# Kernel optimization log

Hardware: AMD Instinct MI355X
Metric: run time of the kernel (lower is better)

Reference implementation:

```python
import math
import jax, jax.numpy as jnp
import numpy as np

NH, D, MULT, VOCAB, NLAYER = 4, 256, 128, 256, 2
N = MULT * D // NH  # 8192
EPS = 1e-5
THETA = 2.0 ** 16


def get_freqs(n):
    q = (jnp.arange(n, dtype=jnp.float32) // 2) * 2  # quantize(t, 2)
    return 1.0 / (THETA ** (q / n)) / (2 * math.pi)


def ln(x):
    # LayerNorm over last dim, no affine
    mu = jnp.mean(x, axis=-1, keepdims=True)
    var = jnp.mean((x - mu) ** 2, axis=-1, keepdims=True)
    return (x - mu) / jnp.sqrt(var + EPS)


def rope(phases, v):
    # phases: (T, N), v: (B, nh, T, N)
    ph = (phases % 1.0) * (2 * math.pi)
    c, s = jnp.cos(ph), jnp.sin(ph)
    v_rot = jnp.stack((-v[..., 1::2], v[..., ::2]), axis=-1).reshape(v.shape)
    return v * c + v_rot * s


def setup_inputs() -> dict:
    key = jax.random.key(0)
    ks = jax.random.split(key, 6)
    std = 0.02
    return {
        "idx": jax.random.randint(ks[0], (1, 2048), 0, VOCAB),
        "embed": jax.random.normal(ks[1], (VOCAB, D), jnp.float32) * std,
        "encoder": jax.random.normal(ks[2], (NH, D, N), jnp.float32) * std,
        "encoder_v": jax.random.normal(ks[3], (NH, D, N), jnp.float32) * std,
        "decoder": jax.random.normal(ks[4], (NH * N, D), jnp.float32) * std,
        "lm_head": jax.random.normal(ks[5], (D, VOCAB), jnp.float32) * std,
    }


def reference(idx, embed, encoder, encoder_v, decoder, lm_head):
    B, T = idx.shape
    freqs = get_freqs(N)  # (N,)
    phases = jnp.arange(T, dtype=jnp.float32)[:, None] * freqs[None, :]  # (T, N)
    # strictly-lower-triangular causal mask (tril diagonal=-1)
    t = jnp.arange(T)
    mask = (t[:, None] > t[None, :]).astype(jnp.float32)  # (T, T)

    x = ln(embed[idx][:, None])  # (B, 1, T, D)
    for _ in range(NLAYER):
        x_sparse = jax.nn.relu(jnp.einsum('bltd,hdn->bhtn', x, encoder))  # (B,nh,T,N)
        QR = rope(phases, x_sparse)
        scores = jnp.einsum('bhtn,bhsn->bhts', QR, QR) * mask  # (B,nh,T,T)
        yKV = ln(jnp.einsum('bhts,blsd->bhtd', scores, x))  # (B,nh,T,D)
        y_sparse = jax.nn.relu(jnp.einsum('bhtd,hdn->bhtn', yKV, encoder_v))
        xy = x_sparse * y_sparse  # (B,nh,T,N)
        xy = xy.transpose(0, 2, 1, 3).reshape(B, 1, T, NH * N)
        yMLP = xy @ decoder  # (B,1,T,D)
        x = ln(x + ln(yMLP))
    logits = x[:, 0] @ lm_head  # (B,T,vocab)
    return logits
```

## Files before the change

kernel.cpp:

```cpp
#include <hip/hip_runtime.h>
#include <hip/hip_bf16.h>
#include <math.h>

typedef unsigned short u16;
typedef unsigned int u32;
typedef __attribute__((ext_vector_type(8))) short short8;
typedef __attribute__((ext_vector_type(4))) float f32x4;

__device__ __forceinline__ u16 f2b(float f) {
  u32 u = __builtin_bit_cast(u32, f);
  u = (u + 0x7fffu + ((u >> 16) & 1u)) >> 16;
  return (u16)u;
}
__device__ __forceinline__ float b2f(u16 s) {
  return __builtin_bit_cast(float, (u32)s << 16);
}

__device__ __forceinline__ void ld_g2l(const u16* g, u16* l) {
  __builtin_amdgcn_global_load_lds(
      (const __attribute__((address_space(1))) unsigned int*)g,
      (__attribute__((address_space(3))) unsigned int*)l, 16, 0, 0);
}

__device__ __forceinline__ float rope_frev(int n) {
  return exp2f((float)(-(n & ~1)) * (1.0f / 512.0f)) * 0.15915494f;
}
__device__ __forceinline__ void rope_cs_fast(float frev, int t, float& c, float& s) {
  float ph = (float)t * frev;
  ph -= floorf(ph);
#if __has_builtin(__builtin_amdgcn_sinf) && __has_builtin(__builtin_amdgcn_cosf)
  s = __builtin_amdgcn_sinf(ph);
  c = __builtin_amdgcn_cosf(ph);
#else
  __sincosf(ph * 6.2831853f, &s, &c);
#endif
}

__device__ __forceinline__ void gemm_core(
    const u16* __restrict__ A, const u16* __restrict__ B,
    int lda, int ldb, int Klen, int kb, int bm, int bn,
    u16* __restrict__ As, u16* __restrict__ Bs, f32x4 (&acc)[4][4])
{
  int tid = threadIdx.x;
  int w = tid >> 6, lane = tid & 63;
  int srow = (w << 4) + (lane >> 2);
  int scol = (lane & 3) << 3;
  const u16* ga0 = A + (long)(bm * 128 + srow) * lda + kb + scol;
  const u16* ga1 = ga0 + (long)64 * lda;
  const u16* gb0 = B + (long)(bn * 128 + srow) * ldb + kb + scol;
  const u16* gb1 = gb0 + (long)64 * ldb;
  u16* la0 = As + (w << 9);  u16* la1 = la0 + 2048;
  u16* lb0 = Bs + (w << 9);  u16* lb1 = lb0 + 2048;

  int wm = (w >> 1) << 6, wn = (w & 1) << 6;
  int lane15 = lane & 15, quad = lane >> 4;
  const u16* ar = As + (wm + lane15) * 32 + quad * 8;
  const u16* br = Bs + (wn + lane15) * 32 + quad * 8;

#pragma unroll
  for (int i = 0; i < 4; i++)
#pragma unroll
    for (int j = 0; j < 4; j++) { f32x4 z = {0.f, 0.f, 0.f, 0.f}; acc[i][j] = z; }

  for (int k = 0; k < Klen; k += 32) {
    ld_g2l(ga0 + k, la0);
    ld_g2l(ga1 + k, la1);
    ld_g2l(gb0 + k, lb0);
    ld_g2l(gb1 + k, lb1);
    __syncthreads();
    short8 af[4], bfr[4];
#pragma unroll
    for (int mt = 0; mt < 4; mt++) af[mt] = *(const short8*)(ar + mt * 16 * 32);
#pragma unroll
    for (int nt = 0; nt < 4; nt++) bfr[nt] = *(const short8*)(br + nt * 16 * 32);
#pragma unroll
    for (int mt = 0; mt < 4; mt++)
#pragma unroll
      for (int nt = 0; nt < 4; nt++)
        acc[mt][nt] = __builtin_amdgcn_mfma_f32_16x16x32_bf16(af[mt], bfr[nt], acc[mt][nt], 0, 0, 0);
    __syncthreads();
  }
}

template<int EPI>
__global__ __launch_bounds__(256, 2) void gemm_bt(
    const u16* __restrict__ A, const u16* __restrict__ B, void* __restrict__ C,
    int K, int lda, int ldb, int ldc, int nsplits, long aB, long bB, long cB,
    int tri)
{
  __shared__ __align__(16) u16 As[128 * 32];
  __shared__ __align__(16) u16 Bs[128 * 32];
  int bn = blockIdx.x, bm = blockIdx.y;
  int batch = blockIdx.z / nsplits, sp = blockIdx.z % nsplits;
  int Klen = K / nsplits, kb = sp * Klen;
  if (tri) {
    int kend = (bm + 1) * 128;
    if (kb >= kend) return;
    if (kb + Klen > kend) Klen = kend - kb;
  }

  f32x4 acc[4][4];
  gemm_core(A + (long)batch * aB, B + (long)batch * bB, lda, ldb, Klen, kb, bm, bn, As, Bs, acc);

  int lane = threadIdx.x & 63, w = threadIdx.x >> 6;
  int wm = (w >> 1) << 6, wn = (w & 1) << 6;
  int lane15 = lane & 15, quad = lane >> 4;

  float frev[4] = {0.f, 0.f, 0.f, 0.f};
  if (EPI == 1 || EPI == 4) {
#pragma unroll
    for (int nt = 0; nt < 4; nt++)
      frev[nt] = rope_frev(bn * 128 + wn + nt * 16 + lane15);
  }

#pragma unroll
  for (int mt = 0; mt < 4; mt++)
#pragma unroll
    for (int nt = 0; nt < 4; nt++) {
      int gn = bn * 128 + wn + nt * 16 + lane15;
#pragma unroll
      for (int r = 0; r < 4; r++) {
        int gm = bm * 128 + wm + mt * 16 + quad * 4 + r;
        float v = acc[mt][nt][r];
        long ci = (long)batch * cB + (long)gm * ldc + gn;
        if (EPI == 0) {
          ((float*)C)[ci] = v;
        } else if (EPI == 1) {
          float rv = fmaxf(v, 0.f);
          float ro = __shfl_xor(rv, 1);
          float c, s; rope_cs_fast(frev[nt], gm, c, s);
          float out = (gn & 1) ? (rv * c + ro * s) : (rv * c - ro * s);
          ((u16*)C)[ci] = f2b(out);
        } else if (EPI == 3) {
          atomicAdd(&((float*)C)[ci], v);
        } else if (EPI == 4) {
          u16* Cp = (u16*)C;
          float q = b2f(Cp[ci]);
          float qo = __shfl_xor(q, 1);
          float c, s; rope_cs_fast(frev[nt], gm, c, s);
          float xs = (gn & 1) ? (q * c - qo * s) : (q * c + qo * s);
          Cp[ci] = f2b(fmaxf(v, 0.f) * xs);
        }
      }
    }
}

#define SC_BAR   __builtin_amdgcn_s_barrier()
#define SC_LGKM0 asm volatile("s_waitcnt lgkmcnt(0)" ::: "memory")
#define SC_LGKM8 asm volatile("s_waitcnt lgkmcnt(8)" ::: "memory")
#define SC_VMF   do { asm volatile("s_waitcnt vmcnt(4)" ::: "memory"); \
                      __builtin_amdgcn_sched_barrier(0); } while (0)
#define SC_P1    __builtin_amdgcn_s_setprio(1)
#define SC_P0    __builtin_amdgcn_s_setprio(0)

#define DSA(Ab, mh) { \
  _Pragma("unroll") for (int mt = 0; mt < 4; mt++) { \
    aA[mt][0] = *(const short8*)((Ab) + ((mh) * 64 + mt * 16) * 64 + koff0); \
    aA[mt][1] = *(const short8*)((Ab) + ((mh) * 64 + mt * 16) * 64 + koff1); } }

#define DSB(Bb, nh, dst) { \
  _Pragma("unroll") for (int nt = 0; nt < 2; nt++) { \
    dst[nt][0] = *(const short8*)((Bb) + ((nh) * 32 + nt * 16) * 64 + koff0); \
    dst[nt][1] = *(const short8*)((Bb) + ((nh) * 32 + nt * 16) * 64 + koff1); } }

#define MMA(MH, NH, BB) { \
  _Pragma("unroll") for (int mt = 0; mt < 4; mt++) \
  _Pragma("unroll") for (int nt = 0; nt < 2; nt++) { \
    acc[(MH)*4+mt][(NH)*2+nt] = __builtin_amdgcn_mfma_f32_16x16x32_bf16( \
        aA[mt][0], BB[nt][0], acc[(MH)*4+mt][(NH)*2+nt], 0, 0, 0); \
    acc[(MH)*4+mt][(NH)*2+nt] = __builtin_amdgcn_mfma_f32_16x16x32_bf16( \
        aA[mt][1], BB[nt][1], acc[(MH)*4+mt][(NH)*2+nt], 0, 0, 0); } }

__global__ __launch_bounds__(512, 1) void gemm_scores8(
    const u16* __restrict__ QR, u16* __restrict__ S, int T)
{
  __shared__ __align__(16) u16 Abuf[2][256 * 64];
  __shared__ __align__(16) u16 Bbuf[2][256 * 64];

  int q = blockIdx.x;
  int bm = (int)((sqrtf(8.f * (float)q + 1.f) - 1.f) * 0.5f);
  while ((bm + 1) * (bm + 2) / 2 <= q) bm++;
  while (bm * (bm + 1) / 2 > q) bm--;
  int bn = q - bm * (bm + 1) / 2;

  const u16* Q = QR + (long)blockIdx.z * (long)T * 8192;
  u16* Sb = S + (long)blockIdx.z * (long)T * T;

  int tid = threadIdx.x;
  int w = tid >> 6, lane = tid & 63;
  int wr = w >> 2, wc = w & 3;
  int lane15 = lane & 15, quad = lane >> 4;
  int swz = lane15 & 7;
  int koff0 = ((quad) ^ swz) << 3;
  int koff1 = ((4 + quad) ^ swz) << 3;

  const u16* gA = Q + (long)(bm * 256) * 8192;
  const u16* gB = Q + (long)(bn * 256) * 8192;

  const u16* A0 = &Abuf[0][(wr * 128 + lane15) * 64];
  const u16* A1 = &Abuf[1][(wr * 128 + lane15) * 64];
  const u16* B0 = &Bbuf[0][(wc * 64 + lane15) * 64];
  const u16* B1 = &Bbuf[1][(wc * 64 + lane15) * 64];

  int sr = lane >> 3, sc = lane & 7;
  long g_sk = (long)sr * 8192 + ((sc ^ sr) << 3);
  int l_base = (w * 16) * 64;
  long g_wrow = (long)(w * 16) * 8192;

  auto STG = [&](const u16* gHalfBase, u16* lHalfBase, int kt) {
    const u16* g = gHalfBase + g_wrow + g_sk + kt * 64;
    u16* l = lHalfBase + l_base;
    ld_g2l(g, l);
    ld_g2l(g + (long)8 * 8192, l + 8 * 64);
  };

  f32x4 acc[8][4];
#pragma unroll
  for (int i2 = 0; i2 < 8; i2++)
#pragma unroll
    for (int j = 0; j < 4; j++) { f32x4 z = {0.f, 0.f, 0.f, 0.f}; acc[i2][j] = z; }

  const long HSTEP = (long)128 * 8192;

  STG(gA, &Abuf[0][0], 0); STG(gA + HSTEP, &Abuf[0][128 * 64], 0);
  STG(gB, &Bbuf[0][0], 0); STG(gB + HSTEP, &Bbuf[0][128 * 64], 0);
  STG(gB, &Bbuf[1][0], 1); STG(gB + HSTEP, &Bbuf[1][128 * 64], 1);
  SC_VMF;
  SC_BAR;

  const int nkt = 8192 / 64;
  for (int i = 0; i < nkt / 2; i++) {
    int kt1 = 2 * i + 1;
    int kt2 = 2 * i + 2; if (kt2 > nkt - 1) kt2 = nkt - 1;
    int kt3 = 2 * i + 3; if (kt3 > nkt - 1) kt3 = nkt - 1;
    short8 aA[4][2], bb0[2][2], bb1[2][2];

    DSA(A0, 0); DSB(B0, 0, bb0);
    STG(gA, &Abuf[1][0], kt1);
    SC_LGKM8; SC_BAR; SC_LGKM0; SC_P1; MMA(0, 0, bb0); SC_P0; SC_BAR;
    DSB(B0, 1, bb1);
    STG(gA + HSTEP, &Abuf[1][128 * 64], kt1);
    SC_BAR; SC_LGKM0; SC_P1; MMA(0, 1, bb1); SC_P0; SC_BAR;
    DSA(A0, 1);
    STG(gB, &Bbuf[0][0], kt2);
    SC_BAR; SC_LGKM0; SC_P1; MMA(1, 1, bb1); SC_P0; SC_BAR;
    STG(gB + HSTEP, &Bbuf[0][128 * 64], kt2);
    SC_VMF; SC_BAR; SC_LGKM0; SC_P1; MMA(1, 0, bb0); SC_P0; SC_BAR;

    DSA(A1, 0); DSB(B1, 0, bb0);
    STG(gA, &Abuf[0][0], kt2);
    SC_LGKM8; SC_BAR; SC_LGKM0; SC_P1; MMA(0, 0, bb0); SC_P0; SC_BAR;
    DSB(B1, 1, bb1);
    STG(gA + HSTEP, &Abuf[0][128 * 64], kt2);
    SC_BAR; SC_LGKM0; SC_P1; MMA(0, 1, bb1); SC_P0; SC_BAR;
    DSA(A1, 1);
    STG(gB, &Bbuf[1][0], kt3);
    SC_BAR; SC_LGKM0; SC_P1; MMA(1, 1, bb1); SC_P0; SC_BAR;
    STG(gB + HSTEP, &Bbuf[1][128 * 64], kt3);
    SC_VMF; SC_BAR; SC_LGKM0; SC_P1; MMA(1, 0, bb0); SC_P0; SC_BAR;
  }

#pragma unroll
  for (int mt = 0; mt < 8; mt++)
#pragma unroll
    for (int nt = 0; nt < 4; nt++) {
      int gn = bn * 256 + wc * 64 + nt * 16 + lane15;
#pragma unroll
      for (int r = 0; r < 4; r++) {
        int gm = bm * 256 + wr * 128 + mt * 16 + quad * 4 + r;
        Sb[(long)gm * T + gn] = f2b(gm > gn ? acc[mt][nt][r] : 0.f);
      }
    }
}

__global__ __launch_bounds__(256) void trans_f32_bf16(
    const float* __restrict__ src, u16* __restrict__ dst, int R, int C)
{
  __shared__ float tile[32][33];
  long off = (long)blockIdx.z * R * C;
  const float* s = src + off;
  u16* d = dst + off;
  int lx = threadIdx.x & 31, ly = threadIdx.x >> 5;
  int c = blockIdx.x * 32 + lx;
#pragma unroll
  for (int p = 0; p < 32; p += 8)
    tile[ly + p][lx] = s[(long)(blockIdx.y * 32 + ly + p) * C + c];
  __syncthreads();
  int rr = blockIdx.y * 32 + lx;
#pragma unroll
  for (int p = 0; p < 32; p += 8)
    d[(long)(blockIdx.x * 32 + ly + p) * R + rr] = f2b(tile[lx][ly + p]);
}

__device__ __forceinline__ float block_sum(float v, float* red) {
#pragma unroll
  for (int o = 32; o > 0; o >>= 1) v += __shfl_down(v, o, 64);
  int lane = threadIdx.x & 63, wid = threadIdx.x >> 6;
  if (lane == 0) red[wid] = v;
  __syncthreads();
  float r = red[0] + red[1] + red[2] + red[3];
  __syncthreads();
  return r;
}

__global__ __launch_bounds__(256) void embed_ln(
    const int* __restrict__ idx, const float* __restrict__ embed,
    float* __restrict__ x, u16* __restrict__ xb, u16* __restrict__ xT, int T)
{
  __shared__ float red[4];
  int t = blockIdx.x, d = threadIdx.x;
  float v = embed[(long)idx[t] * 256 + d];
  float mu = block_sum(v, red) * (1.f / 256.f);
  float c = v - mu;
  float var = block_sum(c * c, red) * (1.f / 256.f);
  float o = c * rsqrtf(var + 1e-5f);
  x[(long)t * 256 + d] = o;
  xb[(long)t * 256 + d] = f2b(o);
  xT[(long)d * T + t] = f2b(o);
}

__global__ __launch_bounds__(256) void row_ln(
    const float* __restrict__ in, u16* __restrict__ out)
{
  __shared__ float red[4];
  long row = blockIdx.x;
  int d = threadIdx.x;
  float v = in[row * 256 + d];
  float mu = block_sum(v, red) * (1.f / 256.f);
  float c = v - mu;
  float var = block_sum(c * c, red) * (1.f / 256.f);
  out[row * 256 + d] = f2b(c * rsqrtf(var + 1e-5f));
}

__global__ __launch_bounds__(256) void resid_ln(
    const float* __restrict__ yMLP, float* __restrict__ x,
    u16* __restrict__ xb, u16* __restrict__ xT, int T)
{
  __shared__ float red[4];
  int t = blockIdx.x, d = threadIdx.x;
  float y = yMLP[(long)t * 256 + d];
  float mu1 = block_sum(y, red) * (1.f / 256.f);
  float c1 = y - mu1;
  float var1 = block_sum(c1 * c1, red) * (1.f / 256.f);
  float l1 = c1 * rsqrtf(var1 + 1e-5f);
  float v = x[(long)t * 256 + d] + l1;
  float mu2 = block_sum(v, red) * (1.f / 256.f);
  float c2 = v - mu2;
  float var2 = block_sum(c2 * c2, red) * (1.f / 256.f);
  float o = c2 * rsqrtf(var2 + 1e-5f);
  x[(long)t * 256 + d] = o;
  xb[(long)t * 256 + d] = f2b(o);
  xT[(long)d * T + t] = f2b(o);
}

extern "C" void kernel_launch(void* const* d_in, const int* in_sizes, int n_in,
                              void* d_out, int out_size, void* d_ws, size_t ws_size,
                              hipStream_t stream) {
  const int*   idx       = (const int*)d_in[0];
  const float* embed     = (const float*)d_in[1];
  const float* encoder   = (const float*)d_in[2];
  const float* encoder_v = (const float*)d_in[3];
  const float* decoder   = (const float*)d_in[4];
  const float* lm_head   = (const float*)d_in[5];
  const int T = in_sizes[0];
  const int D = 256, NH = 4, Nn = 8192, V = 256;

  char* ws = (char*)d_ws;
  size_t off = 0;
  auto alloc = [&](size_t bytes) -> void* {
    void* p = ws + off; off += (bytes + 255) & ~(size_t)255; return p;
  };
  float* x_f32   = (float*)alloc((size_t)T * D * 4);
  float* yMLP    = (float*)alloc((size_t)T * D * 4);
  float* yKV_f32 = (float*)alloc((size_t)NH * T * D * 4);
  u16* x_b    = (u16*)alloc((size_t)T * D * 2);
  u16* xT     = (u16*)alloc((size_t)T * D * 2);
  u16* yKV_b  = (u16*)alloc((size_t)NH * T * D * 2);
  u16* lmT    = (u16*)alloc((size_t)D * V * 2);
  u16* encT   = (u16*)alloc((size_t)NH * Nn * D * 2);
  u16* encvT  = (u16*)alloc((size_t)NH * Nn * D * 2);
  u16* decT   = (u16*)alloc((size_t)D * NH * Nn * 2);
  size_t per_head = ((size_t)T * T * 2 + 256) + ((size_t)T * Nn * 2 + 256);
  int HB = 4;
  while (HB > 1 && off + (size_t)HB * per_head > ws_size) HB >>= 1;
  u16* scores = (u16*)alloc((size_t)HB * T * T * 2);
  u16* QRxy   = (u16*)alloc((size_t)HB * T * Nn * 2);
  if (off > ws_size) return;

  trans_f32_bf16<<<dim3(Nn / 32, D / 32, NH), 256, 0, stream>>>(encoder, encT, D, Nn);
  trans_f32_bf16<<<dim3(Nn / 32, D / 32, NH), 256, 0, stream>>>(encoder_v, encvT, D, Nn);
  trans_f32_bf16<<<dim3(D / 32, (NH * Nn) / 32, 1), 256, 0, stream>>>(decoder, decT, NH * Nn, D);
  trans_f32_bf16<<<dim3(V / 32, D / 32, 1), 256, 0, stream>>>(lm_head, lmT, D, V);

  embed_ln<<<T, 256, 0, stream>>>(idx, embed, x_f32, x_b, xT, T);

  const int nbm = T / 256, ntri = nbm * (nbm + 1) / 2;

  for (int l = 0; l < 2; l++) {
    hipMemsetAsync(yMLP, 0, (size_t)T * D * 4, stream);
    for (int h0 = 0; h0 < NH; h0 += HB) {
      gemm_bt<1><<<dim3(Nn / 128, T / 128, HB), 256, 0, stream>>>(
          x_b, encT + (size_t)h0 * Nn * D, QRxy,
          D, D, D, Nn, 1, 0L, (long)Nn * D, (long)T * Nn, 0);
      gemm_scores8<<<dim3(ntri, 1, HB), 512, 0, stream>>>(QRxy, scores, T);
      hipMemsetAsync(yKV_f32, 0, (size_t)HB * T * D * 4, stream);
      gemm_bt<3><<<dim3(D / 128, T / 128, HB * 8), 256, 0, stream>>>(
          scores, xT, yKV_f32,
          T, T, T, D, 8, (long)T * T, 0L, (long)T * D, 1);
      row_ln<<<HB * T, 256, 0, stream>>>(yKV_f32, yKV_b);
      gemm_bt<4><<<dim3(Nn / 128, T / 128, HB), 256, 0, stream>>>(
          yKV_b, encvT + (size_t)h0 * Nn * D, QRxy,
          D, D, D, Nn, 1, (long)T * D, (long)Nn * D, (long)T * Nn, 0);
      gemm_bt<3><<<dim3(D / 128, T / 128, HB * 8), 256, 0, stream>>>(
          QRxy, decT + (size_t)h0 * Nn, yMLP,
          Nn, Nn, NH * Nn, D, 8, (long)T * Nn, (long)Nn, 0L, 0);
    }
    resid_ln<<<T, 256, 0, stream>>>(yMLP, x_f32, x_b, xT, T);
  }

  gemm_bt<0><<<dim3(V / 128, T / 128, 1), 256, 0, stream>>>(
      x_b, lmT, d_out, D, D, D, V, 1, 0L, 0L, 0L, 0);
}
```

Measured before the change: 1.209 ms.

## Add dedicated K=256 GEMM kernel loading full tiles into LDS for encoder projections

Adds a specialised gemm_k256 kernel for the two encoder projections, where K is exactly 256. Each 512-thread block loads the whole 128x256 A and B tiles into LDS once, using an XOR swizzle, then runs all eight k-steps of MFMA with no further synchronisation. The generic gemm_bt loses its rope/relu epilogues, which move into the new kernel. This removes the per-k-step load/barrier pipeline for these GEMMs. The cost is 128 KB of LDS per block and one block per CU, so global loads are no longer overlapped with compute inside a block.

```diff
diff --git a/kernel.cpp b/kernel.cpp
--- a/kernel.cpp
+++ b/kernel.cpp
@@ -106,13 +106,6 @@
   int wm = (w >> 1) << 6, wn = (w & 1) << 6;
   int lane15 = lane & 15, quad = lane >> 4;
 
-  float frev[4] = {0.f, 0.f, 0.f, 0.f};
-  if (EPI == 1 || EPI == 4) {
-#pragma unroll
-    for (int nt = 0; nt < 4; nt++)
-      frev[nt] = rope_frev(bn * 128 + wn + nt * 16 + lane15);
-  }
-
 #pragma unroll
   for (int mt = 0; mt < 4; mt++)
 #pragma unroll
@@ -125,14 +118,85 @@
         long ci = (long)batch * cB + (long)gm * ldc + gn;
         if (EPI == 0) {
           ((float*)C)[ci] = v;
-        } else if (EPI == 1) {
+        } else if (EPI == 3) {
+          atomicAdd(&((float*)C)[ci], v);
+        }
+      }
+    }
+}
+
+template<int EPI>
+__global__ __launch_bounds__(512, 1) void gemm_k256(
+    const u16* __restrict__ A, const u16* __restrict__ B, void* __restrict__ C,
+    int ldc, long aB, long bB, long cB)
+{
+  __shared__ __align__(16) u16 As[128 * 256];
+  __shared__ __align__(16) u16 Bs[128 * 256];
+
+  int bn = blockIdx.x, bm = blockIdx.y, batch = blockIdx.z;
+  const u16* gA = A + (long)batch * aB + (long)(bm * 128) * 256;
+  const u16* gB = B + (long)batch * bB + (long)(bn * 128) * 256;
+
+  int tid = threadIdx.x, w = tid >> 6, lane = tid & 63;
+  int sr2 = lane >> 5, sc2 = lane & 31;
+
+#pragma unroll
+  for (int j = 0; j < 8; j++) {
+    int row = w * 16 + j * 2 + sr2;
+    int koff = (sc2 ^ (row & 7)) << 3;
+    ld_g2l(gA + (long)row * 256 + koff, As + (w * 16 + j * 2) * 256);
+    ld_g2l(gB + (long)row * 256 + koff, Bs + (w * 16 + j * 2) * 256);
+  }
+  __syncthreads();
+
+  int wr = w >> 2, wc = w & 3;
+  int lane15 = lane & 15, quad = lane >> 4;
+  int swz = lane15 & 7;
+  const u16* aRow = As + (wr * 64 + lane15) * 256;
+  const u16* bRow = Bs + (wc * 32 + lane15) * 256;
+
+  f32x4 acc[4][2];
+#pragma unroll
+  for (int i = 0; i < 4; i++)
+#pragma unroll
+    for (int j = 0; j < 2; j++) { f32x4 z = {0.f, 0.f, 0.f, 0.f}; acc[i][j] = z; }
+
+#pragma unroll
+  for (int kstep = 0; kstep < 8; kstep++) {
+    int koffk = ((kstep * 4 + quad) ^ swz) << 3;
+    short8 af[4], bfr[2];
+#pragma unroll
+    for (int mt = 0; mt < 4; mt++) af[mt] = *(const short8*)(aRow + mt * 16 * 256 + koffk);
+#pragma unroll
+    for (int nt = 0; nt < 2; nt++) bfr[nt] = *(const short8*)(bRow + nt * 16 * 256 + koffk);
+#pragma unroll
+    for (int mt = 0; mt < 4; mt++)
+#pragma unroll
+      for (int nt = 0; nt < 2; nt++)
+        acc[mt][nt] = __builtin_amdgcn_mfma_f32_16x16x32_bf16(af[mt], bfr[nt], acc[mt][nt], 0, 0, 0);
+  }
+
+  float frev[2];
+#pragma unroll
+  for (int nt = 0; nt < 2; nt++)
+    frev[nt] = rope_frev(bn * 128 + wc * 32 + nt * 16 + lane15);
+
+#pragma unroll
+  for (int mt = 0; mt < 4; mt++)
+#pragma unroll
+    for (int nt = 0; nt < 2; nt++) {
+      int gn = bn * 128 + wc * 32 + nt * 16 + lane15;
+#pragma unroll
+      for (int r = 0; r < 4; r++) {
+        int gm = bm * 128 + wr * 64 + mt * 16 + quad * 4 + r;
+        float v = acc[mt][nt][r];
+        long ci = (long)batch * cB + (long)gm * ldc + gn;
+        if (EPI == 1) {
           float rv = fmaxf(v, 0.f);
           float ro = __shfl_xor(rv, 1);
           float c, s; rope_cs_fast(frev[nt], gm, c, s);
           float out = (gn & 1) ? (rv * c + ro * s) : (rv * c - ro * s);
           ((u16*)C)[ci] = f2b(out);
-        } else if (EPI == 3) {
-          atomicAdd(&((float*)C)[ci], v);
         } else if (EPI == 4) {
           u16* Cp = (u16*)C;
           float q = b2f(Cp[ci]);
@@ -399,18 +463,18 @@
   for (int l = 0; l < 2; l++) {
     hipMemsetAsync(yMLP, 0, (size_t)T * D * 4, stream);
     for (int h0 = 0; h0 < NH; h0 += HB) {
-      gemm_bt<1><<<dim3(Nn / 128, T / 128, HB), 256, 0, stream>>>(
+      gemm_k256<1><<<dim3(Nn / 128, T / 128, HB), 512, 0, stream>>>(
           x_b, encT + (size_t)h0 * Nn * D, QRxy,
-          D, D, D, Nn, 1, 0L, (long)Nn * D, (long)T * Nn, 0);
+          Nn, 0L, (long)Nn * D, (long)T * Nn);
       gemm_scores8<<<dim3(ntri, 1, HB), 512, 0, stream>>>(QRxy, scores, T);
       hipMemsetAsync(yKV_f32, 0, (size_t)HB * T * D * 4, stream);
       gemm_bt<3><<<dim3(D / 128, T / 128, HB * 8), 256, 0, stream>>>(
           scores, xT, yKV_f32,
           T, T, T, D, 8, (long)T * T, 0L, (long)T * D, 1);
       row_ln<<<HB * T, 256, 0, stream>>>(yKV_f32, yKV_b);
-      gemm_bt<4><<<dim3(Nn / 128, T / 128, HB), 256, 0, stream>>>(
+      gemm_k256<4><<<dim3(Nn / 128, T / 128, HB), 512, 0, stream>>>(
           yKV_b, encvT + (size_t)h0 * Nn * D, QRxy,
-          D, D, D, Nn, 1, (long)T * D, (long)Nn * D, (long)T * Nn, 0);
+          Nn, (long)T * D, (long)Nn * D, (long)T * Nn);
       gemm_bt<3><<<dim3(D / 128, T / 128, HB * 8), 256, 0, stream>>>(
           QRxy, decT + (size_t)h0 * Nn, yMLP,
           Nn, Nn, NH * Nn, D, 8, (long)T * Nn, (long)Nn, 0L, 0);
```

Result: slower. 1.385 ms (+14.5%).
